# Performance work log

Measured on AMD Instinct MI355X. Metric: run time of the kernel, lower is better.

The kernel has to match this reference:

```python
import jax, jax.numpy as jnp
import numpy as np

IN_C, OUT_C, N = 512, 256, 8192
NEG_INF = -1000000000.0  # matches torch's -1e9 fill


def setup_inputs() -> dict:
    key = jax.random.key(0)
    ks = jax.random.split(key, 8)
    x = jax.random.normal(ks[0], (N, IN_C), dtype=jnp.float32)
    adj = jax.random.randint(ks[1], (N, N), 0, 2, dtype=jnp.int32)
    # fc: Linear(in_c, out_c)
    lim_fc = 1.0 / np.sqrt(IN_C)
    W_fc = jax.random.uniform(ks[2], (IN_C, OUT_C), minval=-lim_fc, maxval=lim_fc, dtype=jnp.float32)
    b_fc = jax.random.uniform(ks[3], (OUT_C,), minval=-lim_fc, maxval=lim_fc, dtype=jnp.float32)
    # a1, a2: Linear(out_c, 1)
    lim_a = 1.0 / np.sqrt(OUT_C)
    W_a1 = jax.random.uniform(ks[4], (OUT_C, 1), minval=-lim_a, maxval=lim_a, dtype=jnp.float32)
    b_a1 = jax.random.uniform(ks[5], (1,), minval=-lim_a, maxval=lim_a, dtype=jnp.float32)
    W_a2 = jax.random.uniform(ks[6], (OUT_C, 1), minval=-lim_a, maxval=lim_a, dtype=jnp.float32)
    b_a2 = jax.random.uniform(ks[7], (1,), minval=-lim_a, maxval=lim_a, dtype=jnp.float32)
    return {"x": x, "adj": adj, "W_fc": W_fc, "b_fc": b_fc,
            "W_a1": W_a1, "b_a1": b_a1, "W_a2": W_a2, "b_a2": b_a2}


def reference(x, adj, W_fc, b_fc, W_a1, b_a1, W_a2, b_a2):
    h = x @ W_fc + b_fc                      # [N, out_c]
    s1 = h @ W_a1 + b_a1                     # [N, 1]
    s2 = h @ W_a2 + b_a2                     # [N, 1]
    e = jax.nn.leaky_relu(s1 + s2.T)         # [N, N], slope 0.01 matches torch default
    att = jnp.where(adj > 0, e, NEG_INF)
    att = jax.nn.softmax(att, axis=1)        # dropout omitted (eval mode)
    return att @ h                           # [N, out_c]
```

## Files before the change

### kernel.cpp

```cpp
#include <hip/hip_runtime.h>
#include <hip/hip_bf16.h>

#define IN_C 512
#define OUT_C 256
#define NN 8192
#define JSPL 4
#define JRANGE (NN / JSPL)
#define NT (JRANGE / 32)

typedef __attribute__((ext_vector_type(8))) short s16x8;
typedef __attribute__((ext_vector_type(4))) float f32x4;

__device__ __forceinline__ ushort f2bf(float f) {
    unsigned u = __float_as_uint(f);
    unsigned r = (u + 0x7FFF + ((u >> 16) & 1)) >> 16;
    return (ushort)r;
}

__device__ __forceinline__ void gload_lds16(const uint4* g, uint4* l) {
    __builtin_amdgcn_global_load_lds(
        (const __attribute__((address_space(1))) unsigned int*)g,
        (__attribute__((address_space(3))) unsigned int*)l, 16, 0, 0);
}

__global__ __launch_bounds__(256) void fc_kernel(
    const float* __restrict__ x, const float* __restrict__ Wfc,
    const float* __restrict__ bfc, const float* __restrict__ Wa1,
    const float* __restrict__ ba1, const float* __restrict__ Wa2,
    const float* __restrict__ ba2,
    uint4* __restrict__ hb,
    float* __restrict__ s1, float* __restrict__ s2)
{
    __shared__ float xl[8 * IN_C];
    __shared__ float red[2][8][4];
    const int t = threadIdx.x;
    const int r0 = blockIdx.x * 8;

    {
        const float4* src = (const float4*)(x + (size_t)r0 * IN_C);
        float4* dst = (float4*)xl;
        #pragma unroll
        for (int i = 0; i < 4; i++) dst[i * 256 + t] = src[i * 256 + t];
    }
    __syncthreads();

    float acc[8];
    #pragma unroll
    for (int r = 0; r < 8; r++) acc[r] = 0.f;

    for (int c4 = 0; c4 < IN_C / 4; c4++) {
        const float w0 = Wfc[(c4 * 4 + 0) * OUT_C + t];
        const float w1 = Wfc[(c4 * 4 + 1) * OUT_C + t];
        const float w2 = Wfc[(c4 * 4 + 2) * OUT_C + t];
        const float w3 = Wfc[(c4 * 4 + 3) * OUT_C + t];
        #pragma unroll
        for (int r = 0; r < 8; r++) {
            const float4 xv = *(const float4*)&xl[r * IN_C + c4 * 4];
            acc[r] = fmaf(xv.x, w0, acc[r]);
            acc[r] = fmaf(xv.y, w1, acc[r]);
            acc[r] = fmaf(xv.z, w2, acc[r]);
            acc[r] = fmaf(xv.w, w3, acc[r]);
        }
    }
    const float bb = bfc[t];
    #pragma unroll
    for (int r = 0; r < 8; r++) acc[r] += bb;

    {
        union { ushort u[8]; uint4 v; } pk;
        #pragma unroll
        for (int r = 0; r < 8; r++) pk.u[r] = f2bf(acc[r]);
        const int jt = r0 >> 5, u = (r0 >> 3) & 3;
        hb[(size_t)jt * 1024 + u * 256 + t] = pk.v;
    }

    float p1[8], p2[8];
    const float wa1 = Wa1[t], wa2 = Wa2[t];
    #pragma unroll
    for (int r = 0; r < 8; r++) { p1[r] = acc[r] * wa1; p2[r] = acc[r] * wa2; }
    #pragma unroll
    for (int off = 32; off > 0; off >>= 1) {
        #pragma unroll
        for (int r = 0; r < 8; r++) {
            p1[r] += __shfl_down(p1[r], off);
            p2[r] += __shfl_down(p2[r], off);
        }
    }
    const int wv = t >> 6, ln = t & 63;
    if (ln == 0) {
        #pragma unroll
        for (int r = 0; r < 8; r++) { red[0][r][wv] = p1[r]; red[1][r][wv] = p2[r]; }
    }
    __syncthreads();
    if (t < 16) {
        const int s = t >> 3, r = t & 7;
        float v = red[s][r][0] + red[s][r][1] + red[s][r][2] + red[s][r][3];
        v += s ? ba2[0] : ba1[0];
        if (s) s2[r0 + r] = v; else s1[r0 + r] = v;
    }
}

__global__ __launch_bounds__(256) void smax_kernel(const float* __restrict__ s2,
                                                   float* __restrict__ smax)
{
    __shared__ float red[4];
    float m = -1e30f;
    for (int i = threadIdx.x; i < NN; i += 256) m = fmaxf(m, s2[i]);
    #pragma unroll
    for (int off = 32; off > 0; off >>= 1) m = fmaxf(m, __shfl_down(m, off));
    if ((threadIdx.x & 63) == 0) red[threadIdx.x >> 6] = m;
    __syncthreads();
    if (threadIdx.x == 0)
        smax[0] = fmaxf(fmaxf(red[0], red[1]), fmaxf(red[2], red[3]));
}

__global__ __launch_bounds__(256, 2) void attn_kernel(
    const int* __restrict__ adj, const uint4* __restrict__ hb,
    const float* __restrict__ s1, const float* __restrict__ s2,
    const float* __restrict__ smaxp, float* __restrict__ outp,
    float* __restrict__ pbase, float* __restrict__ rs)
{
    __shared__ float s2l[JRANGE];
    __shared__ uint4 hbuf[2][1024];
    __shared__ unsigned long long mask_lds[64][33];

    const int t = threadIdx.x;
    const int wave = t >> 6, lane = t & 63;
    const int g = lane >> 4, lr = lane & 15;
    const int jq = blockIdx.y;
    const int Jbase = jq * JRANGE;
    const int R0 = blockIdx.x * 64;
    const int row = R0 + wave * 16 + lr;

    const uint4* hb_base = hb + (size_t)(Jbase >> 5) * 1024;

    #pragma unroll
    for (int q = 0; q < 4; q++)
        gload_lds16(hb_base + q * 256 + t, &hbuf[0][q * 256 + t]);

    {
        const float4* src = (const float4*)(s2 + Jbase);
        float4* dst = (float4*)s2l;
        #pragma unroll
        for (int i = 0; i < JRANGE / 4 / 256; i++) dst[i * 256 + t] = src[i * 256 + t];
    }

    {
        const int* abase = adj + (size_t)(R0 + wave * 16) * NN + Jbase + lane;
        for (int c = 0; c < 32; ++c) {
            int v[16];
            #pragma unroll
            for (int r = 0; r < 16; ++r)
                v[r] = __builtin_nontemporal_load(abase + (size_t)r * NN + c * 64);
            #pragma unroll
            for (int r = 0; r < 16; ++r) {
                const unsigned long long m = __ballot(v[r] > 0);
                if (lane == 0) mask_lds[wave * 16 + r][c] = m;
            }
        }
    }
    __syncthreads();

    const float my_s1 = s1[row];
    const float z0 = my_s1 + smaxp[0];
    const float m_i = fmaxf(z0, 0.01f * z0);

    f32x4 acc[16];
    #pragma unroll
    for (int n = 0; n < 16; n++) acc[n] = (f32x4)(0.f);
    float rsum = 0.f;

    for (int tt = 0; tt < NT; ++tt) {
        const int cur = tt & 1;
        const bool more = (tt + 1 < NT);
        if (more) {
            const uint4* gs = hb_base + (size_t)(tt + 1) * 1024;
            #pragma unroll
            for (int q = 0; q < 4; q++)
                gload_lds16(gs + q * 256 + t, &hbuf[cur ^ 1][q * 256 + t]);
        }

        const unsigned long long m64 = mask_lds[wave * 16 + lr][tt >> 1];
        const unsigned mb = (unsigned)(m64 >> ((tt & 1) * 32 + g * 8)) & 0xFFu;

        const int j0 = tt * 32 + g * 8;
        const float4 sva = *(const float4*)(s2l + j0);
        const float4 svb = *(const float4*)(s2l + j0 + 4);
        const float sv[8] = {sva.x, sva.y, sva.z, sva.w, svb.x, svb.y, svb.z, svb.w};
        union { ushort u[8]; s16x8 v; } pk;
        #pragma unroll
        for (int e = 0; e < 8; e++) {
            const float zz = my_s1 + sv[e];
            const float ee = fmaxf(zz, 0.01f * zz);
            float p = __expf(ee - m_i);
            p = ((mb >> e) & 1u) ? p : 0.f;
            rsum += p;
            pk.u[e] = f2bf(p);
        }
        const s16x8 afrag = pk.v;
        #pragma unroll
        for (int n = 0; n < 16; n++) {
            const s16x8 bfrag = *(const s16x8*)&hbuf[cur][g * 256 + n * 16 + lr];
            acc[n] = __builtin_amdgcn_mfma_f32_16x16x32_bf16(afrag, bfrag, acc[n], 0, 0, 0);
        }
        __syncthreads();
    }

    rsum += __shfl_xor(rsum, 16);
    rsum += __shfl_xor(rsum, 32);
    if (g == 0) rs[(size_t)jq * NN + row] = rsum;

    float* dst = (jq == 0) ? outp : (pbase + (size_t)(jq - 1) * ((size_t)NN * OUT_C));
    #pragma unroll
    for (int r = 0; r < 4; r++) {
        const int orow = R0 + wave * 16 + g * 4 + r;
        float* op = dst + (size_t)orow * OUT_C + lr;
        #pragma unroll
        for (int n = 0; n < 16; n++) op[n * 16] = acc[n][r];
    }
}

__global__ __launch_bounds__(256) void combine_kernel(
    float* __restrict__ out, const float* __restrict__ pbase,
    const float* __restrict__ rs)
{
    const int row = blockIdx.x, t = threadIdx.x;
    const float rsum = rs[row] + rs[NN + row] + rs[2 * NN + row] + rs[3 * NN + row];
    const float inv = 1.f / rsum;
    const size_t idx = (size_t)row * OUT_C + t;
    const size_t stride = (size_t)NN * OUT_C;
    const float v = out[idx] + pbase[idx] + pbase[idx + stride] + pbase[idx + 2 * stride];
    out[idx] = v * inv;
}

extern "C" void kernel_launch(void* const* d_in, const int* in_sizes, int n_in,
                              void* d_out, int out_size, void* d_ws, size_t ws_size,
                              hipStream_t stream) {
    const float* x   = (const float*)d_in[0];
    const int*   adj = (const int*)d_in[1];
    const float* Wfc = (const float*)d_in[2];
    const float* bfc = (const float*)d_in[3];
    const float* Wa1 = (const float*)d_in[4];
    const float* ba1 = (const float*)d_in[5];
    const float* Wa2 = (const float*)d_in[6];
    const float* ba2 = (const float*)d_in[7];
    float* out = (float*)d_out;

    char* ws = (char*)d_ws;
    uint4* hb   = (uint4*)ws;
    float* s1   = (float*)(ws + (4u << 20));
    float* s2   = s1 + NN;
    float* rs   = s2 + NN;
    float* smax = rs + 4 * NN;
    float* pbase = (float*)(ws + (5u << 20));

    fc_kernel<<<dim3(NN / 8), 256, 0, stream>>>(x, Wfc, bfc, Wa1, ba1, Wa2, ba2, hb, s1, s2);
    smax_kernel<<<dim3(1), 256, 0, stream>>>(s2, smax);
    attn_kernel<<<dim3(NN / 64, JSPL), 256, 0, stream>>>(adj, hb, s1, s2, smax, out, pbase, rs);
    combine_kernel<<<dim3(NN), 256, 0, stream>>>(out, pbase, rs);
}
```

Before: 189.4 us.

## Split attention over 8 column chunks and read h fragments directly from global

```diff
diff --git a/kernel.cpp b/kernel.cpp
--- a/kernel.cpp
+++ b/kernel.cpp
@@ -4,9 +4,10 @@
 #define IN_C 512
 #define OUT_C 256
 #define NN 8192
-#define JSPL 4
+#define JSPL 8
 #define JRANGE (NN / JSPL)
 #define NT (JRANGE / 32)
+#define L2E 1.44269504088896f
 
 typedef __attribute__((ext_vector_type(8))) short s16x8;
 typedef __attribute__((ext_vector_type(4))) float f32x4;
@@ -15,12 +16,6 @@
     unsigned u = __float_as_uint(f);
     unsigned r = (u + 0x7FFF + ((u >> 16) & 1)) >> 16;
     return (ushort)r;
-}
-
-__device__ __forceinline__ void gload_lds16(const uint4* g, uint4* l) {
-    __builtin_amdgcn_global_load_lds(
-        (const __attribute__((address_space(1))) unsigned int*)g,
-        (__attribute__((address_space(3))) unsigned int*)l, 16, 0, 0);
 }
 
 __global__ __launch_bounds__(256) void fc_kernel(
@@ -114,15 +109,14 @@
         smax[0] = fmaxf(fmaxf(red[0], red[1]), fmaxf(red[2], red[3]));
 }
 
-__global__ __launch_bounds__(256, 2) void attn_kernel(
+__global__ __launch_bounds__(256, 4) void attn_kernel(
     const int* __restrict__ adj, const uint4* __restrict__ hb,
     const float* __restrict__ s1, const float* __restrict__ s2,
     const float* __restrict__ smaxp, float* __restrict__ outp,
     float* __restrict__ pbase, float* __restrict__ rs)
 {
     __shared__ float s2l[JRANGE];
-    __shared__ uint4 hbuf[2][1024];
-    __shared__ unsigned long long mask_lds[64][33];
+    __shared__ unsigned long long mask_lds[64][16];
 
     const int t = threadIdx.x;
     const int wave = t >> 6, lane = t & 63;
@@ -132,37 +126,33 @@
     const int R0 = blockIdx.x * 64;
     const int row = R0 + wave * 16 + lr;
 
-    const uint4* hb_base = hb + (size_t)(Jbase >> 5) * 1024;
-
-    #pragma unroll
-    for (int q = 0; q < 4; q++)
-        gload_lds16(hb_base + q * 256 + t, &hbuf[0][q * 256 + t]);
-
     {
         const float4* src = (const float4*)(s2 + Jbase);
         float4* dst = (float4*)s2l;
-        #pragma unroll
-        for (int i = 0; i < JRANGE / 4 / 256; i++) dst[i * 256 + t] = src[i * 256 + t];
-    }
-
-    {
-        const int* abase = adj + (size_t)(R0 + wave * 16) * NN + Jbase + lane;
-        for (int c = 0; c < 32; ++c) {
+        const float4 v = src[t];
+        dst[t] = make_float4(v.x * L2E, v.y * L2E, v.z * L2E, v.w * L2E);
+    }
+
+    {
+        const int wrow0 = wave * 16;
+        for (int r = 0; r < 16; ++r) {
+            const int* arow = adj + (size_t)(R0 + wrow0 + r) * NN + Jbase + lane;
             int v[16];
             #pragma unroll
-            for (int r = 0; r < 16; ++r)
-                v[r] = __builtin_nontemporal_load(abase + (size_t)r * NN + c * 64);
+            for (int c = 0; c < 16; ++c)
+                v[c] = __builtin_nontemporal_load(arow + c * 64);
+            unsigned long long myw = 0;
             #pragma unroll
-            for (int r = 0; r < 16; ++r) {
-                const unsigned long long m = __ballot(v[r] > 0);
-                if (lane == 0) mask_lds[wave * 16 + r][c] = m;
+            for (int c = 0; c < 16; ++c) {
+                const unsigned long long m = __ballot(v[c] > 0);
+                if (lane == c) myw = m;
             }
-        }
-    }
-    __syncthreads();
-
-    const float my_s1 = s1[row];
-    const float z0 = my_s1 + smaxp[0];
+            if (lane < 16) mask_lds[wrow0 + r][lane] = myw;
+        }
+    }
+
+    const float my_s1 = s1[row] * L2E;
+    const float z0 = my_s1 + smaxp[0] * L2E;
     const float m_i = fmaxf(z0, 0.01f * z0);
 
     f32x4 acc[16];
@@ -170,16 +160,11 @@
     for (int n = 0; n < 16; n++) acc[n] = (f32x4)(0.f);
     float rsum = 0.f;
 
+    const uint4* hb_base = hb + (size_t)(Jbase >> 5) * 1024;
+
+    __syncthreads();
+
     for (int tt = 0; tt < NT; ++tt) {
-        const int cur = tt & 1;
-        const bool more = (tt + 1 < NT);
-        if (more) {
-            const uint4* gs = hb_base + (size_t)(tt + 1) * 1024;
-            #pragma unroll
-            for (int q = 0; q < 4; q++)
-                gload_lds16(gs + q * 256 + t, &hbuf[cur ^ 1][q * 256 + t]);
-        }
-
         const unsigned long long m64 = mask_lds[wave * 16 + lr][tt >> 1];
         const unsigned mb = (unsigned)(m64 >> ((tt & 1) * 32 + g * 8)) & 0xFFu;
 
@@ -192,18 +177,25 @@
         for (int e = 0; e < 8; e++) {
             const float zz = my_s1 + sv[e];
             const float ee = fmaxf(zz, 0.01f * zz);
-            float p = __expf(ee - m_i);
+            float p = exp2f(ee - m_i);
             p = ((mb >> e) & 1u) ? p : 0.f;
             rsum += p;
             pk.u[e] = f2bf(p);
         }
         const s16x8 afrag = pk.v;
-        #pragma unroll
-        for (int n = 0; n < 16; n++) {
-            const s16x8 bfrag = *(const s16x8*)&hbuf[cur][g * 256 + n * 16 + lr];
-            acc[n] = __builtin_amdgcn_mfma_f32_16x16x32_bf16(afrag, bfrag, acc[n], 0, 0, 0);
-        }
-        __syncthreads();
+
+        const uint4* bsrc = hb_base + (size_t)tt * 1024 + g * 256 + lr;
+        uint4 bf[8];
+        #pragma unroll
+        for (int n = 0; n < 8; n++) bf[n] = bsrc[n * 16];
+        #pragma unroll
+        for (int n = 0; n < 8; n++)
+            acc[n] = __builtin_amdgcn_mfma_f32_16x16x32_bf16(afrag, *(const s16x8*)&bf[n], acc[n], 0, 0, 0);
+        #pragma unroll
+        for (int n = 0; n < 8; n++) bf[n] = bsrc[128 + n * 16];
+        #pragma unroll
+        for (int n = 0; n < 8; n++)
+            acc[n + 8] = __builtin_amdgcn_mfma_f32_16x16x32_bf16(afrag, *(const s16x8*)&bf[n], acc[n + 8], 0, 0, 0);
     }
 
     rsum += __shfl_xor(rsum, 16);
@@ -216,7 +208,8 @@
         const int orow = R0 + wave * 16 + g * 4 + r;
         float* op = dst + (size_t)orow * OUT_C + lr;
         #pragma unroll
-        for (int n = 0; n < 16; n++) op[n * 16] = acc[n][r];
+        for (int n = 0; n < 16; n++)
+            __builtin_nontemporal_store(acc[n][r], op + n * 16);
     }
 }
 
@@ -225,11 +218,16 @@
     const float* __restrict__ rs)
 {
     const int row = blockIdx.x, t = threadIdx.x;
-    const float rsum = rs[row] + rs[NN + row] + rs[2 * NN + row] + rs[3 * NN + row];
+    float rsum = 0.f;
+    #pragma unroll
+    for (int q = 0; q < JSPL; q++) rsum += rs[(size_t)q * NN + row];
     const float inv = 1.f / rsum;
     const size_t idx = (size_t)row * OUT_C + t;
     const size_t stride = (size_t)NN * OUT_C;
-    const float v = out[idx] + pbase[idx] + pbase[idx + stride] + pbase[idx + 2 * stride];
+    float v = out[idx];
+    #pragma unroll
+    for (int q = 0; q < JSPL - 1; q++)
+        v += __builtin_nontemporal_load(&pbase[idx + (size_t)q * stride]);
     out[idx] = v * inv;
 }
 
@@ -251,7 +249,7 @@
     float* s1   = (float*)(ws + (4u << 20));
     float* s2   = s1 + NN;
     float* rs   = s2 + NN;
-    float* smax = rs + 4 * NN;
+    float* smax = rs + JSPL * NN;
     float* pbase = (float*)(ws + (5u << 20));
 
     fc_kernel<<<dim3(NN / 8), 256, 0, stream>>>(x, Wfc, bfc, Wa1, ba1, Wa2, ba2, hb, s1, s2);
```

Result: slower. 208.6 us (+10.1%).
